# Kernel tuning notes

Measured on AMD Instinct MI355X. Metric: run time of the kernel, lower is better.

## Reference

```python
import jax, jax.numpy as jnp
import numpy as np

B, S, D = 4, 8192, 1024
NC = 5
EPS = 1e-5  # nn.LayerNorm default eps


def setup_inputs() -> dict:
    key = jax.random.key(0)
    kx, kid, kg, kb, ks, kw, kbias = jax.random.split(key, 7)
    x = jax.random.normal(kx, (B, S, D), dtype=jnp.float32)
    compartment_ids = jax.random.randint(kid, (B, S), 0, NC)
    # per-compartment LayerNorm affine params (stacked) and scaling
    gamma = 1.0 + 0.1 * jax.random.normal(kg, (NC, D), dtype=jnp.float32)
    beta = 0.1 * jax.random.normal(kb, (NC, D), dtype=jnp.float32)
    scale = 1.0 + 0.1 * jax.random.normal(ks, (NC,), dtype=jnp.float32)
    # compartment_transition_norm: nn.Linear(d_model, d_model)
    W = jax.random.normal(kw, (D, D), dtype=jnp.float32) / np.sqrt(D)
    b = 0.01 * jax.random.normal(kbias, (D,), dtype=jnp.float32)
    return {"x": x, "compartment_ids": compartment_ids, "gamma": gamma,
            "beta": beta, "scale": scale, "W": W, "b": b}


def reference(x, compartment_ids, gamma, beta, scale, W, b):
    # tokens with id >= NC are left untouched (original guard)
    valid = compartment_ids < NC                      # [B,S]
    cid = jnp.clip(compartment_ids, 0, NC - 1)        # safe gather index
    # per-token LayerNorm statistics over last dim (biased variance)
    mu = jnp.mean(x, axis=-1, keepdims=True)
    var = jnp.mean(jnp.square(x - mu), axis=-1, keepdims=True)
    normed = (x - mu) * jax.lax.rsqrt(var + EPS)      # [B,S,D]
    g = gamma[cid]                                    # [B,S,D]
    bt = beta[cid]                                    # [B,S,D]
    s = scale[cid][..., None]                         # [B,S,1]
    y = (normed * g + bt) * s
    y = jnp.where(valid[..., None], y, x)
    # residual transition: x + Linear(x)
    return y + jnp.einsum('bsd,ed->bse', y, W) + b
```

## Files before the change

kernel.cpp:

```cpp
#include <hip/hip_runtime.h>
#include <stdint.h>

#define NCOMP 5
#define DM 1024
#define LN_EPS 1e-5f

typedef __attribute__((ext_vector_type(8))) __bf16 bf16x8;
typedef __attribute__((ext_vector_type(4))) float f32x4;

__device__ __forceinline__ unsigned short f2bf(float f) {
    unsigned u = __builtin_bit_cast(unsigned, f);
    u += 0x7fffu + ((u >> 16) & 1u);
    return (unsigned short)(u >> 16);
}

__global__ __launch_bounds__(128) void ln_w_kernel(
    const float* __restrict__ x, const int* __restrict__ cid,
    const float* __restrict__ gamma, const float* __restrict__ beta,
    const float* __restrict__ scale, const float* __restrict__ W,
    unsigned short* __restrict__ y, unsigned short* __restrict__ Wb, int M)
{
    const int tid = threadIdx.x;
    __shared__ float red[8];
    const int base = blockIdx.x * 4;
#pragma unroll
    for (int u = 0; u < 4; u++) {
        const int t = base + u;
        if (t < M) {
            const float* xp = x + (size_t)t * DM + tid * 8;
            const float4 a = *(const float4*)xp;
            const float4 b = *(const float4*)(xp + 4);
            float s  = a.x + a.y + a.z + a.w + b.x + b.y + b.z + b.w;
            float ss = a.x*a.x + a.y*a.y + a.z*a.z + a.w*a.w
                     + b.x*b.x + b.y*b.y + b.z*b.z + b.w*b.w;
#pragma unroll
            for (int off = 32; off > 0; off >>= 1) {
                s  += __shfl_down(s, off);
                ss += __shfl_down(ss, off);
            }
            float* rr = red + (u & 1) * 4;
            if ((tid & 63) == 0) { rr[tid >> 6] = s; rr[2 + (tid >> 6)] = ss; }
            __syncthreads();
            const float mu  = (rr[0] + rr[1]) * (1.0f / DM);
            const float var = (rr[2] + rr[3]) * (1.0f / DM) - mu * mu;
            const float rs  = rsqrtf(var + LN_EPS);
            const int craw  = cid[t];
            const bool valid = craw < NCOMP;
            const int c = min(max(craw, 0), NCOMP - 1);
            const float sc = scale[c];
            const float* gp = gamma + c * DM + tid * 8;
            const float* bp = beta  + c * DM + tid * 8;
            const float4 g0 = *(const float4*)gp;
            const float4 g1 = *(const float4*)(gp + 4);
            const float4 b0 = *(const float4*)bp;
            const float4 b1 = *(const float4*)(bp + 4);
            float o[8];
            o[0] = valid ? ((a.x - mu) * rs * g0.x + b0.x) * sc : a.x;
            o[1] = valid ? ((a.y - mu) * rs * g0.y + b0.y) * sc : a.y;
            o[2] = valid ? ((a.z - mu) * rs * g0.z + b0.z) * sc : a.z;
            o[3] = valid ? ((a.w - mu) * rs * g0.w + b0.w) * sc : a.w;
            o[4] = valid ? ((b.x - mu) * rs * g1.x + b1.x) * sc : b.x;
            o[5] = valid ? ((b.y - mu) * rs * g1.y + b1.y) * sc : b.y;
            o[6] = valid ? ((b.z - mu) * rs * g1.z + b1.z) * sc : b.z;
            o[7] = valid ? ((b.w - mu) * rs * g1.w + b1.w) * sc : b.w;
            uint4 p;
            p.x = (unsigned)f2bf(o[0]) | ((unsigned)f2bf(o[1]) << 16);
            p.y = (unsigned)f2bf(o[2]) | ((unsigned)f2bf(o[3]) << 16);
            p.z = (unsigned)f2bf(o[4]) | ((unsigned)f2bf(o[5]) << 16);
            p.w = (unsigned)f2bf(o[6]) | ((unsigned)f2bf(o[7]) << 16);
            *(uint4*)(y + (size_t)t * DM + tid * 8) = p;
        } else {
            const int row = t - M;
            const float* wp = W + (size_t)row * DM + tid * 8;
            const float4 a = *(const float4*)wp;
            const float4 b = *(const float4*)(wp + 4);
            float o[8] = {a.x, a.y, a.z, a.w, b.x, b.y, b.z, b.w};
            const int d = row - tid * 8;
            if (d >= 0 && d < 8) o[d] += 1.0f;
            uint4 p;
            p.x = (unsigned)f2bf(o[0]) | ((unsigned)f2bf(o[1]) << 16);
            p.y = (unsigned)f2bf(o[2]) | ((unsigned)f2bf(o[3]) << 16);
            p.z = (unsigned)f2bf(o[4]) | ((unsigned)f2bf(o[5]) << 16);
            p.w = (unsigned)f2bf(o[6]) | ((unsigned)f2bf(o[7]) << 16);
            *(uint4*)(Wb + (size_t)row * DM + tid * 8) = p;
        }
    }
}

__device__ __forceinline__ void gld_lds16(const unsigned short* g, unsigned short* l) {
    __builtin_amdgcn_global_load_lds(
        (const __attribute__((address_space(1))) unsigned int*)(uintptr_t)g,
        (__attribute__((address_space(3))) unsigned int*)(uintptr_t)l,
        16, 0, 0);
}

__global__ __launch_bounds__(256) void gemm_kernel(
    const unsigned short* __restrict__ A,
    const unsigned short* __restrict__ Bp,
    const float* __restrict__ bias,
    float* __restrict__ C, int M)
{
    constexpr int K = 1024, N = 1024, BK = 32, TM = 128, NIT = K / BK;
    __shared__ __align__(16) unsigned short smem[16384];

    const int tid  = threadIdx.x;
    const int bm   = blockIdx.x * TM;
    const int bn   = blockIdx.y * TM;
    const int lane = tid & 63;
    const int wave = tid >> 6;
    const int wm   = (wave >> 1) * 64;
    const int wn   = (wave & 1) * 64;

    const int r0 = tid >> 2;
    const int c0 = (tid & 3) * 8;
    const unsigned short* Ag  = A  + (size_t)(bm + r0) * K + c0;
    const unsigned short* Ag2 = A  + (size_t)(bm + 64 + r0) * K + c0;
    const unsigned short* Bg  = Bp + (size_t)(bn + r0) * K + c0;
    const unsigned short* Bg2 = Bp + (size_t)(bn + 64 + r0) * K + c0;

    f32x4 acc[4][4] = {};
    const int quad = lane >> 4;
    const int qk = quad * 8;
    const int fr = lane & 15;

    {
        unsigned short* s = smem;
        gld_lds16(Ag, s + (size_t)tid * 8);
        gld_lds16(Ag2, s + (size_t)(tid + 256) * 8);
        gld_lds16(Bg, s + 4096 + (size_t)tid * 8);
        gld_lds16(Bg2, s + 4096 + (size_t)(tid + 256) * 8);
    }
    __syncthreads();

#pragma unroll 2
    for (int i = 0; i < NIT; i++) {
        if (i + 1 < NIT) {
            const int kn = (i + 1) * BK;
            unsigned short* s = smem + ((i + 1) & 1) * 8192;
            gld_lds16(Ag  + kn, s + (size_t)tid * 8);
            gld_lds16(Ag2 + kn, s + (size_t)(tid + 256) * 8);
            gld_lds16(Bg  + kn, s + 4096 + (size_t)tid * 8);
            gld_lds16(Bg2 + kn, s + 4096 + (size_t)(tid + 256) * 8);
        }
        const unsigned short* As = smem + (i & 1) * 8192;
        const unsigned short* Bs = As + 4096;
        bf16x8 af[4], bfr[4];
#pragma unroll
        for (int j = 0; j < 4; j++)
            af[j] = *(const bf16x8*)&As[(wm + j * 16 + fr) * BK + qk];
#pragma unroll
        for (int j = 0; j < 4; j++)
            bfr[j] = *(const bf16x8*)&Bs[(wn + j * 16 + fr) * BK + qk];
#pragma unroll
        for (int mi = 0; mi < 4; mi++)
#pragma unroll
            for (int ni = 0; ni < 4; ni++)
                acc[mi][ni] = __builtin_amdgcn_mfma_f32_16x16x32_bf16(
                    af[mi], bfr[ni], acc[mi][ni], 0, 0, 0);
        __syncthreads();
    }

    float* tb = (float*)smem + wave * 1088;
    const int erow = lane >> 3;
    const int ecol = (lane & 7) * 4;
    float4 bv0 = *(const float4*)&bias[bn + wn + ecol];
    float4 bv1 = *(const float4*)&bias[bn + wn + 32 + ecol];
#pragma unroll
    for (int mi = 0; mi < 4; mi++) {
#pragma unroll
        for (int ni = 0; ni < 4; ni++)
#pragma unroll
            for (int r = 0; r < 4; r++)
                tb[(quad * 4 + r) * 68 + ni * 16 + fr] = acc[mi][ni][r];
#pragma unroll
        for (int j = 0; j < 4; j++) {
            const int row  = (j >> 1) * 8 + erow;
            const int colg = (j & 1) * 32 + ecol;
            const int gr = bm + wm + mi * 16 + row;
            const float4 v = *(const float4*)&tb[row * 68 + colg];
            const float4 bv = (j & 1) ? bv1 : bv0;
            float4 o;
            o.x = v.x + bv.x; o.y = v.y + bv.y;
            o.z = v.z + bv.z; o.w = v.w + bv.w;
            *(float4*)&C[(size_t)gr * N + bn + wn + colg] = o;
        }
    }
}

extern "C" void kernel_launch(void* const* d_in, const int* in_sizes, int n_in,
                              void* d_out, int out_size, void* d_ws, size_t ws_size,
                              hipStream_t stream)
{
    const float* x     = (const float*)d_in[0];
    const int*   cid   = (const int*)d_in[1];
    const float* gamma = (const float*)d_in[2];
    const float* beta  = (const float*)d_in[3];
    const float* scale = (const float*)d_in[4];
    const float* W     = (const float*)d_in[5];
    const float* bias  = (const float*)d_in[6];
    float* out = (float*)d_out;

    const int M = in_sizes[0] / DM;
    unsigned short* yb = (unsigned short*)d_ws;
    unsigned short* Wb = yb + (size_t)M * DM;

    ln_w_kernel<<<(M + DM) / 4, 128, 0, stream>>>(x, cid, gamma, beta, scale, W, yb, Wb, M);
    dim3 grid(M / 128, DM / 128);
    gemm_kernel<<<grid, 256, 0, stream>>>(yb, Wb, bias, out, M);
}
```

Measured before the change: 345.3 us.

## Restructure GEMM to 256x256 tiles with 4-stage LDS pipeline and swizzle

```diff
diff --git a/kernel.cpp b/kernel.cpp
--- a/kernel.cpp
+++ b/kernel.cpp
@@ -87,93 +87,132 @@
     }
 }
 
-__device__ __forceinline__ void gld_lds16(const unsigned short* g, unsigned short* l) {
+__device__ __forceinline__ void gld16(const unsigned short* g, unsigned short* l) {
     __builtin_amdgcn_global_load_lds(
         (const __attribute__((address_space(1))) unsigned int*)(uintptr_t)g,
         (__attribute__((address_space(3))) unsigned int*)(uintptr_t)l,
         16, 0, 0);
 }
 
-__global__ __launch_bounds__(256) void gemm_kernel(
+__global__ __launch_bounds__(512, 2) void gemm_kernel(
     const unsigned short* __restrict__ A,
     const unsigned short* __restrict__ Bp,
     const float* __restrict__ bias,
     float* __restrict__ C, int M)
 {
-    constexpr int K = 1024, N = 1024, BK = 32, TM = 128, NIT = K / BK;
-    __shared__ __align__(16) unsigned short smem[16384];
+    constexpr int K = 1024, N = 1024;
+    constexpr int BUF = 16384;
+    __shared__ __align__(16) unsigned short smem[4 * BUF];
 
     const int tid  = threadIdx.x;
-    const int bm   = blockIdx.x * TM;
-    const int bn   = blockIdx.y * TM;
     const int lane = tid & 63;
     const int wave = tid >> 6;
-    const int wm   = (wave >> 1) * 64;
-    const int wn   = (wave & 1) * 64;
-
-    const int r0 = tid >> 2;
-    const int c0 = (tid & 3) * 8;
-    const unsigned short* Ag  = A  + (size_t)(bm + r0) * K + c0;
-    const unsigned short* Ag2 = A  + (size_t)(bm + 64 + r0) * K + c0;
-    const unsigned short* Bg  = Bp + (size_t)(bn + r0) * K + c0;
-    const unsigned short* Bg2 = Bp + (size_t)(bn + 64 + r0) * K + c0;
-
-    f32x4 acc[4][4] = {};
+    const int wm   = (wave >> 2) * 128;
+    const int wn   = (wave & 3) * 64;
+
+    const int nwg = gridDim.x;
+    int wg = blockIdx.x;
+    if ((nwg & 7) == 0) wg = (wg & 7) * (nwg >> 3) + (wg >> 3);
+    const int bm = (wg >> 2) * 256;
+    const int bn = (wg & 3) * 256;
+
+    const int qsrc = (((lane & 3) ^ ((lane >> 3) & 3))) * 8;
+    const int rA0  = (wave * 2) * 16 + (lane >> 2);
+    const unsigned short* gA0 = A  + (size_t)(bm + rA0) * K + qsrc;
+    const unsigned short* gA1 = A  + (size_t)(bm + rA0 + 16) * K + qsrc;
+    const unsigned short* gB0 = Bp + (size_t)(bn + rA0) * K + qsrc;
+    const unsigned short* gB1 = Bp + (size_t)(bn + rA0 + 16) * K + qsrc;
+    const int sA0 = (wave * 2) * 512 + lane * 8;
+    const int sA1 = sA0 + 512;
+    const int sB0 = 8192 + sA0;
+    const int sB1 = 8192 + sA1;
+
+    const int fr   = lane & 15;
     const int quad = lane >> 4;
-    const int qk = quad * 8;
-    const int fr = lane & 15;
-
-    {
-        unsigned short* s = smem;
-        gld_lds16(Ag, s + (size_t)tid * 8);
-        gld_lds16(Ag2, s + (size_t)(tid + 256) * 8);
-        gld_lds16(Bg, s + 4096 + (size_t)tid * 8);
-        gld_lds16(Bg2, s + 4096 + (size_t)(tid + 256) * 8);
-    }
-    __syncthreads();
-
-#pragma unroll 2
-    for (int i = 0; i < NIT; i++) {
-        if (i + 1 < NIT) {
-            const int kn = (i + 1) * BK;
-            unsigned short* s = smem + ((i + 1) & 1) * 8192;
-            gld_lds16(Ag  + kn, s + (size_t)tid * 8);
-            gld_lds16(Ag2 + kn, s + (size_t)(tid + 256) * 8);
-            gld_lds16(Bg  + kn, s + 4096 + (size_t)tid * 8);
-            gld_lds16(Bg2 + kn, s + 4096 + (size_t)(tid + 256) * 8);
-        }
-        const unsigned short* As = smem + (i & 1) * 8192;
-        const unsigned short* Bs = As + 4096;
-        bf16x8 af[4], bfr[4];
-#pragma unroll
-        for (int j = 0; j < 4; j++)
-            af[j] = *(const bf16x8*)&As[(wm + j * 16 + fr) * BK + qk];
-#pragma unroll
-        for (int j = 0; j < 4; j++)
-            bfr[j] = *(const bf16x8*)&Bs[(wn + j * 16 + fr) * BK + qk];
-#pragma unroll
-        for (int mi = 0; mi < 4; mi++)
-#pragma unroll
-            for (int ni = 0; ni < 4; ni++)
-                acc[mi][ni] = __builtin_amdgcn_mfma_f32_16x16x32_bf16(
-                    af[mi], bfr[ni], acc[mi][ni], 0, 0, 0);
-        __syncthreads();
+    const int loff = fr * 32 + ((quad ^ ((fr >> 1) & 3)) * 8);
+
+    f32x4 acc[8][4] = {};
+
+#pragma unroll
+    for (int kt = 0; kt < 3; ++kt) {
+        unsigned short* sb = smem + kt * BUF;
+        gld16(gA0 + kt * 32, sb + sA0);
+        gld16(gA1 + kt * 32, sb + sA1);
+        gld16(gB0 + kt * 32, sb + sB0);
+        gld16(gB1 + kt * 32, sb + sB1);
+    }
+    gA0 += 96; gA1 += 96; gB0 += 96; gB1 += 96;
+
+    asm volatile("s_waitcnt vmcnt(8)" ::: "memory");
+    __builtin_amdgcn_s_barrier();
+
+    for (int t = 0; t < 32; ++t) {
+        const unsigned short* Asb = smem + (t & 3) * BUF;
+        const unsigned short* Bsb = Asb + 8192;
+        unsigned short* stg = smem + ((t + 3) & 3) * BUF;
+        const bool do_stage = (t < 29);
+
+        bf16x8 bfr[4], af[4];
+#pragma unroll
+        for (int j = 0; j < 4; ++j)
+            bfr[j] = *(const bf16x8*)&Bsb[(wn + j * 16) * 32 + loff];
+#pragma unroll
+        for (int j = 0; j < 4; ++j)
+            af[j] = *(const bf16x8*)&Asb[(wm + j * 16) * 32 + loff];
+        if (do_stage) {
+            gld16(gA0, stg + sA0);
+            gld16(gA1, stg + sA1);
+        }
+        __builtin_amdgcn_s_barrier();
+        asm volatile("s_waitcnt lgkmcnt(0)" ::: "memory");
+        __builtin_amdgcn_s_setprio(1);
+#pragma unroll
+        for (int j = 0; j < 4; ++j)
+#pragma unroll
+            for (int n = 0; n < 4; ++n)
+                acc[j][n] = __builtin_amdgcn_mfma_f32_16x16x32_bf16(
+                    af[j], bfr[n], acc[j][n], 0, 0, 0);
+        __builtin_amdgcn_s_setprio(0);
+        __builtin_amdgcn_s_barrier();
+
+#pragma unroll
+        for (int j = 0; j < 4; ++j)
+            af[j] = *(const bf16x8*)&Asb[(wm + 64 + j * 16) * 32 + loff];
+        if (do_stage) {
+            gld16(gB0, stg + sB0);
+            gld16(gB1, stg + sB1);
+            gA0 += 32; gA1 += 32; gB0 += 32; gB1 += 32;
+        }
+        if (t < 29)       asm volatile("s_waitcnt vmcnt(8)" ::: "memory");
+        else if (t == 29) asm volatile("s_waitcnt vmcnt(4)" ::: "memory");
+        else              asm volatile("s_waitcnt vmcnt(0)" ::: "memory");
+        __builtin_amdgcn_s_barrier();
+        asm volatile("s_waitcnt lgkmcnt(0)" ::: "memory");
+        __builtin_amdgcn_s_setprio(1);
+#pragma unroll
+        for (int j = 0; j < 4; ++j)
+#pragma unroll
+            for (int n = 0; n < 4; ++n)
+                acc[4 + j][n] = __builtin_amdgcn_mfma_f32_16x16x32_bf16(
+                    af[j], bfr[n], acc[4 + j][n], 0, 0, 0);
+        __builtin_amdgcn_s_setprio(0);
+        __builtin_amdgcn_s_barrier();
     }
 
     float* tb = (float*)smem + wave * 1088;
     const int erow = lane >> 3;
     const int ecol = (lane & 7) * 4;
-    float4 bv0 = *(const float4*)&bias[bn + wn + ecol];
-    float4 bv1 = *(const float4*)&bias[bn + wn + 32 + ecol];
-#pragma unroll
-    for (int mi = 0; mi < 4; mi++) {
-#pragma unroll
-        for (int ni = 0; ni < 4; ni++)
-#pragma unroll
-            for (int r = 0; r < 4; r++)
+    const float4 bv0 = *(const float4*)&bias[bn + wn + ecol];
+    const float4 bv1 = *(const float4*)&bias[bn + wn + 32 + ecol];
+#pragma unroll
+    for (int mi = 0; mi < 8; ++mi) {
+#pragma unroll
+        for (int ni = 0; ni < 4; ++ni)
+#pragma unroll
+            for (int r = 0; r < 4; ++r)
                 tb[(quad * 4 + r) * 68 + ni * 16 + fr] = acc[mi][ni][r];
 #pragma unroll
-        for (int j = 0; j < 4; j++) {
+        for (int j = 0; j < 4; ++j) {
             const int row  = (j >> 1) * 8 + erow;
             const int colg = (j & 1) * 32 + ecol;
             const int gr = bm + wm + mi * 16 + row;
@@ -205,6 +244,5 @@
     unsigned short* Wb = yb + (size_t)M * DM;
 
     ln_w_kernel<<<(M + DM) / 4, 128, 0, stream>>>(x, cid, gamma, beta, scale, W, yb, Wb, M);
-    dim3 grid(M / 128, DM / 128);
-    gemm_kernel<<<grid, 256, 0, stream>>>(yb, Wb, bias, out, M);
-}
+    gemm_kernel<<<dim3((M / 256) * 4), 512, 0, stream>>>(yb, Wb, bias, out, M);
+}
```

After: 325.9 us. 1.06x faster.
